# Optimization experiments

Hardware: AMD Instinct MI355X
Metric: run time of the kernel (lower is better)

The kernel has to match this reference:

```python
import jax, jax.numpy as jnp
import numpy as np

D_MODEL = 2048
N_HEADS = 16
N_KV = 4
HEAD_DIM = 128
SUB = 64
WINDOW = 512
THETA = 10000.0
NEG = jnp.float32(-1e30)


def _rope_tables(seq_len):
    inv_freq = 1.0 / (THETA ** (jnp.arange(0, HEAD_DIM, 2, dtype=jnp.float32) / HEAD_DIM))
    freqs = jnp.arange(seq_len, dtype=jnp.float32)[:, None] * inv_freq[None, :]  # [S, hd/2]
    emb = jnp.concatenate([freqs, freqs], axis=-1)  # [S, hd]
    return jnp.cos(emb), jnp.sin(emb)


def _rotate_half(x):
    x1, x2 = x[..., : HEAD_DIM // 2], x[..., HEAD_DIM // 2 :]
    return jnp.concatenate([-x2, x1], axis=-1)


def _apply_rope(t, cos, sin):
    # t: [B, H, S, hd]; cos/sin: [S, hd]
    c = cos[None, None]
    s = sin[None, None]
    return t * c + _rotate_half(t) * s


def setup_inputs() -> dict:
    key = jax.random.key(0)
    ks = jax.random.split(key, 6)
    B, S = 1, 2048
    std = 0.02
    return {
        "x": jax.random.normal(ks[0], (B, S, D_MODEL), dtype=jnp.float32),
        "Wq": jax.random.normal(ks[1], (D_MODEL, N_HEADS * HEAD_DIM), dtype=jnp.float32) * std,
        "Wk": jax.random.normal(ks[2], (D_MODEL, N_KV * HEAD_DIM), dtype=jnp.float32) * std,
        "Wv": jax.random.normal(ks[3], (D_MODEL, N_KV * HEAD_DIM), dtype=jnp.float32) * std,
        "Wo": jax.random.normal(ks[4], (N_HEADS * HEAD_DIM, D_MODEL), dtype=jnp.float32) * std,
        "lam": jnp.full((N_HEADS,), 0.1, dtype=jnp.float32),
    }


def reference(x, Wq, Wk, Wv, Wo, lam):
    B, S, _ = x.shape
    n_rep = N_HEADS // N_KV

    q = (x @ Wq).reshape(B, S, N_HEADS, HEAD_DIM).transpose(0, 2, 1, 3)  # [B,H,S,hd]
    k = (x @ Wk).reshape(B, S, N_KV, HEAD_DIM).transpose(0, 2, 1, 3)    # [B,KH,S,hd]
    v = (x @ Wv).reshape(B, S, N_KV, HEAD_DIM).transpose(0, 2, 1, 3)

    cos, sin = _rope_tables(S)
    q = _apply_rope(q, cos, sin)
    k = _apply_rope(k, cos, sin)

    # GQA repeat: each kv head replicated n_rep times consecutively
    k = jnp.repeat(k, n_rep, axis=1)  # [B,H,S,hd]
    v = jnp.repeat(v, n_rep, axis=1)

    q1, q2 = q[..., :SUB], q[..., SUB:]
    k1, k2 = k[..., :SUB], k[..., SUB:]
    scale = 1.0 / jnp.sqrt(jnp.float32(SUB))

    s1 = jnp.einsum("bhqd,bhkd->bhqk", q1, k1) * scale
    s2 = jnp.einsum("bhqd,bhkd->bhqk", q2, k2) * scale

    i = jnp.arange(S)[:, None]
    j = jnp.arange(S)[None, :]
    allowed = (j <= i) & (j >= i - WINDOW + 1)  # causal + sliding window
    s1 = jnp.where(allowed[None, None], s1, NEG)
    s2 = jnp.where(allowed[None, None], s2, NEG)

    a1 = jax.nn.softmax(s1.astype(jnp.float32), axis=-1).astype(x.dtype)
    a2 = jax.nn.softmax(s2.astype(jnp.float32), axis=-1).astype(x.dtype)

    diff = jax.nn.relu(a1 - lam[None, :, None, None] * a2)
    diff = diff / (jnp.sum(diff, axis=-1, keepdims=True) + 1e-6)

    out = jnp.einsum("bhqk,bhkd->bhqd", diff, v)  # [B,H,S,hd]
    out = out.transpose(0, 2, 1, 3).reshape(B, S, N_HEADS * HEAD_DIM)
    return out @ Wo
```

## Files before the change

kernel.cpp:

```cpp
#include <hip/hip_runtime.h>
#include <hip/hip_bf16.h>
#include <stdint.h>

typedef __attribute__((ext_vector_type(8))) short short8;
typedef __attribute__((ext_vector_type(4))) float f32x4;
using bf16 = __hip_bfloat16;

#define MFMA16(a, b, c) __builtin_amdgcn_mfma_f32_16x16x32_bf16((a), (b), (c), 0, 0, 0)

#define GLOAD_LDS16(g, l) __builtin_amdgcn_global_load_lds( \
    (const __attribute__((address_space(1))) void*)(g),     \
    (__attribute__((address_space(3))) void*)(l), 16, 0, 0)

__device__ __forceinline__ unsigned packbf2(float lo, float hi) {
  unsigned r;
  asm("v_cvt_pk_bf16_f32 %0, %1, %2" : "=v"(r) : "v"(lo), "v"(hi));
  return r;
}
__device__ __forceinline__ float ex2(float x) {
  float r;
  asm("v_exp_f32 %0, %1" : "=v"(r) : "v"(x));
  return r;
}
__device__ __forceinline__ float bflo(unsigned a) {
  union { unsigned u; float f; } v; v.u = a << 16; return v.f;
}
__device__ __forceinline__ float bfhi(unsigned a) {
  union { unsigned u; float f; } v; v.u = a & 0xFFFF0000u; return v.f;
}

template <bool EDGE, bool STORE>
__device__ __forceinline__ void p1v(const f32x4* s1v, const f32x4* s2v,
                                    float& l1, float& l2,
                                    int kb0, int myq, int lhi, int qrow,
                                    unsigned* Pt) {
  float sum1 = 0.f, sum2 = 0.f;
#pragma unroll
  for (int nt = 0; nt < 4; ++nt) {
#pragma unroll
    for (int r = 0; r < 4; ++r) {
      float e1 = ex2(s1v[nt][r]);
      float e2 = ex2(s2v[nt][r]);
      if (EDGE) {
        int key = kb0 + nt * 16 + lhi * 4 + r;
        bool ok = (key <= myq) && (key > myq - 512);
        e1 = ok ? e1 : 0.f;
        e2 = ok ? e2 : 0.f;
      }
      sum1 += e1; sum2 += e2;
      if (STORE)
        Pt[(nt * 16 + lhi * 4 + r) * 64 + qrow] = packbf2(e1, e2);
    }
  }
  l1 += sum1; l2 += sum2;
}

template <bool EDGE>
__device__ __forceinline__ float p2s(const f32x4* s1v, const f32x4* s2v,
                                     float c2, int kb0, int myq, int lhi, int l15,
                                     unsigned* pw) {
  float d0 = 0.f, d1 = 0.f;
#pragma unroll
  for (int nt = 0; nt < 4; ++nt) {
    float pr[4];
#pragma unroll
    for (int r = 0; r < 4; ++r) {
      float e1 = ex2(s1v[nt][r]);
      float e2 = ex2(s2v[nt][r]);
      float p = fmaf(-c2, e2, e1);
      p = fmaxf(p, 0.f);
      if (EDGE) {
        int key = kb0 + nt * 16 + lhi * 4 + r;
        bool ok = (key <= myq) && (key > myq - 512);
        p = ok ? p : 0.f;
      }
      pr[r] = p;
      if (r & 1) d1 += p; else d0 += p;
    }
    int pi = l15 * 36 + 8 * nt + 2 * lhi;
    pw[pi]     = packbf2(pr[0], pr[1]);
    pw[pi + 1] = packbf2(pr[2], pr[3]);
  }
  return d0 + d1;
}

__global__ __launch_bounds__(256) void prep_all(const float* __restrict__ x,
                                                const float* __restrict__ Wq,
                                                const float* __restrict__ Wk,
                                                const float* __restrict__ Wv,
                                                const float* __restrict__ Wo,
                                                bf16* __restrict__ xb,
                                                bf16* __restrict__ WqkvFT,
                                                bf16* __restrict__ WoFT)
{
  const int bx = blockIdx.x;
  const int tid = threadIdx.x;
  if (bx >= 80) {
    size_t i = ((size_t)(bx - 80) * 32 + blockIdx.y) * 2048 + tid * 8;
    const float* f = x + i;
    float4 a = *(const float4*)f;
    float4 b = *(const float4*)(f + 4);
    union { bf16 h[8]; short8 s; } u;
    u.h[0] = __float2bfloat16(a.x); u.h[1] = __float2bfloat16(a.y);
    u.h[2] = __float2bfloat16(a.z); u.h[3] = __float2bfloat16(a.w);
    u.h[4] = __float2bfloat16(b.x); u.h[5] = __float2bfloat16(b.y);
    u.h[6] = __float2bfloat16(b.z); u.h[7] = __float2bfloat16(b.w);
    *(short8*)(xb + i) = u.s;
    return;
  }
  const float* W;
  bf16* Wt;
  int N, n0, prm;
  if (bx < 32)      { W = Wq; Wt = WqkvFT; N = 2048; n0 = bx * 64;               prm = 1; }
  else if (bx < 40) { W = Wk; Wt = WqkvFT; N = 512;  n0 = 2048 + (bx - 32) * 64; prm = 1; }
  else if (bx < 48) { W = Wv; Wt = WqkvFT; N = 512;  n0 = 2560 + (bx - 40) * 64; prm = 0; }
  else              { W = Wo; Wt = WoFT;   N = 2048; n0 = (bx - 48) * 64;        prm = 0; }
  const int nloc0 = (N == 512) ? (n0 - ((n0 >= 2560) ? 2560 : 2048)) : ((bx < 32 || bx >= 48) ? (n0 & 2047) : 0);
  const int k0 = blockIdx.y * 64;

  __shared__ bf16 t[64][72];
#pragma unroll
  for (int pass = 0; pass < 4; ++pass) {
    int r = pass * 16 + (tid >> 4);
    int c = (tid & 15) * 4;
    float4 v = *(const float4*)(W + (size_t)(k0 + r) * N + nloc0 + c);
    t[c + 0][r] = __float2bfloat16(v.x);
    t[c + 1][r] = __float2bfloat16(v.y);
    t[c + 2][r] = __float2bfloat16(v.z);
    t[c + 3][r] = __float2bfloat16(v.w);
  }
  __syncthreads();
#pragma unroll
  for (int pass = 0; pass < 2; ++pass) {
    int n = pass * 32 + (tid >> 3);
    int k8 = (tid & 7) * 8;
    int ng = n0 + n;
    if (prm) {
      int d = ng & 127;
      int dp = (d & 31) | ((d & 32) << 1) | ((d & 64) >> 1);
      ng = (ng & ~127) | dp;
    }
    int frag = (ng >> 4) * 64 + ((k0 + k8) >> 5);
    int ln = (ng & 15) + 16 * ((k8 >> 3) & 3);
    *(short8*)(Wt + (size_t)frag * 512 + ln * 8) = *(const short8*)(&t[n][k8]);
  }
}

__global__ __launch_bounds__(512) void gemm_qkv(const bf16* __restrict__ A,
                                                const bf16* __restrict__ Bft,
                                                bf16* __restrict__ QKV,
                                                bf16* __restrict__ VTp,
                                                int M, int N, int K)
{
  __shared__ __align__(16) char smem[65536];
  bf16* As = (bf16*)smem;

  const int tid  = threadIdx.x;
  const int lane = tid & 63;
  const int w    = tid >> 6;
  const int wmg  = (w >> 2) * 4;
  const int wn3  = (w & 3) * 3;
  const int l15  = lane & 15;
  const int lhi  = lane >> 4;

  const int nbx = gridDim.x;
  const int lb  = blockIdx.y * nbx + blockIdx.x;
  const int nwg = nbx * gridDim.y;
  const int lsw = (lb & 7) * (nwg >> 3) + (lb >> 3);
  const int bm0 = (lsw / nbx) * 128;
  const int bn0 = (lsw % nbx) * 192;

  const int srow = tid >> 2;
  const int scol = ((tid & 3) ^ ((tid >> 3) & 3)) * 8;
  const int loff = l15 * 4 + (lhi ^ ((l15 >> 1) & 3));

  const int nkc = K >> 5;
  const bf16* bbase[3];
#pragma unroll
  for (int nt = 0; nt < 3; ++nt)
    bbase[nt] = Bft + ((size_t)((bn0 >> 4) + wn3 + nt) * nkc) * 512 + lane * 8;

  f32x4 acc[4][3];
  const f32x4 zero4 = {0.f, 0.f, 0.f, 0.f};
#pragma unroll
  for (int i = 0; i < 4; ++i)
#pragma unroll
    for (int j = 0; j < 3; ++j) acc[i][j] = zero4;

  short8 br0[3], br1[3], br2[3], br3[3];

#define GSTAGE_A(buf, kk)                                                           \
  { GLOAD_LDS16(A + (size_t)(bm0 + srow) * K + (kk) + scol,                         \
                As + (buf) * 4096 + tid * 8); }

#define BLOAD(breg, kc)                                                             \
  { _Pragma("unroll")                                                               \
    for (int nt = 0; nt < 3; ++nt) {                                                \
      asm volatile("global_load_dwordx4 %0, %1, off"                                \
                   : "=v"(breg[nt])                                                 \
                   : "v"(bbase[nt] + (size_t)(kc) * 512)                            \
                   : "memory");                                                     \
    } }

#define KSTEP(aslot, breg, wcn, ...)                                                \
  {                                                                                 \
    asm volatile("s_waitcnt vmcnt(" #wcn ")" ::: "memory");                         \
    __builtin_amdgcn_s_barrier();                                                   \
    __builtin_amdgcn_sched_barrier(0);                                              \
    __VA_ARGS__                                                                     \
    short8 a_[4];                                                                   \
    _Pragma("unroll")                                                               \
    for (int mt = 0; mt < 4; ++mt)                                                  \
      a_[mt] = *(const short8*)(As + (aslot) * 4096 + ((wmg + mt) * 64 + loff) * 8);\
    _Pragma("unroll")                                                               \
    for (int mt = 0; mt < 4; ++mt)                                                  \
      _Pragma("unroll")                                                             \
      for (int nt = 0; nt < 3; ++nt)                                                \
        acc[mt][nt] = MFMA16(a_[mt], breg[nt], acc[mt][nt]);                        \
  }

  GSTAGE_A(0, 0);  BLOAD(br0, 0);
  GSTAGE_A(1, 32); BLOAD(br1, 1);
  GSTAGE_A(2, 64); BLOAD(br2, 2);

  for (int t = 0; t < nkc - 4; t += 4) {
    KSTEP(0, br0, 8, GSTAGE_A(3, (t + 3) * 32); BLOAD(br3, t + 3);)
    KSTEP(1, br1, 8, GSTAGE_A(0, (t + 4) * 32); BLOAD(br0, t + 4);)
    KSTEP(2, br2, 8, GSTAGE_A(1, (t + 5) * 32); BLOAD(br1, t + 5);)
    KSTEP(3, br3, 8, GSTAGE_A(2, (t + 6) * 32); BLOAD(br2, t + 6);)
  }
  KSTEP(0, br0, 8, GSTAGE_A(3, (nkc - 1) * 32); BLOAD(br3, nkc - 1);)
  KSTEP(1, br1, 8, )
  KSTEP(2, br2, 4, )
  KSTEP(3, br3, 0, )
#undef GSTAGE_A
#undef BLOAD
#undef KSTEP

  __syncthreads();

  const int ropeW = (bn0 + 192 <= 2560) ? 192 : ((bn0 >= 2560) ? 0 : 64);

  if (ropeW > 0) {
    float* Lf = (float*)smem;
#pragma unroll
    for (int half = 0; half < 2; ++half) {
      if ((w >> 2) == half) {
#pragma unroll
        for (int mt = 0; mt < 4; ++mt)
#pragma unroll
          for (int nt = 0; nt < 3; ++nt) {
            int lc = (wn3 + nt) * 16 + l15;
            if (lc < ropeW) {
#pragma unroll
              for (int r = 0; r < 4; ++r)
                Lf[(mt * 16 + lhi * 4 + r) * ropeW + lc] = acc[mt][nt][r];
            }
          }
      }
      __syncthreads();
      {
        int row = tid >> 3;
        int s = bm0 + half * 64 + row;
        if (ropeW == 192) {
          int cg = (tid & 7) * 24;
          bf16* orow = QKV + (size_t)s * 3072 + bn0 + cg;
          union { bf16 h[24]; short8 v[3]; } o;
#pragma unroll
          for (int e = 0; e < 24; ++e) {
            int c = cg + e;
            int g = bn0 + c;
            int p = g & 127;
            int w32 = p & 63;
            int b = p >> 6;
            int d = b * 32 + (w32 & 31);
            float scale = (g < 2048) ? 0.180336880111120f : 1.0f;
            float inv = __expf(-(float)d * (9.210340371976184f / 64.0f));
            float ang = (float)s * inv;
            float cs = __cosf(ang), sn = __sinf(ang);
            bool first = (w32 < 32);
            float xa = Lf[row * 192 + c];
            float xb2 = Lf[row * 192 + (first ? c + 32 : c - 32)];
            float out = fmaf(first ? -xb2 : xb2, sn, xa * cs);
            o.h[e] = __float2bfloat16(out * scale);
          }
          *(short8*)(orow)      = o.v[0];
          *(short8*)(orow + 8)  = o.v[1];
          *(short8*)(orow + 16) = o.v[2];
        } else {
          int cg = (tid & 7) * 8;
          bf16* orow = QKV + (size_t)s * 3072 + bn0 + cg;
          union { bf16 h[8]; short8 v; } o;
#pragma unroll
          for (int e = 0; e < 8; ++e) {
            int c = cg + e;
            int g = bn0 + c;
            int p = g & 127;
            int w32 = p & 63;
            int b = p >> 6;
            int d = b * 32 + (w32 & 31);
            float inv = __expf(-(float)d * (9.210340371976184f / 64.0f));
            float ang = (float)s * inv;
            float cs = __cosf(ang), sn = __sinf(ang);
            bool first = (w32 < 32);
            float xa = Lf[row * 64 + c];
            float xb2 = Lf[row * 64 + (first ? c + 32 : c - 32)];
            float out = fmaf(first ? -xb2 : xb2, sn, xa * cs);
            o.h[e] = __float2bfloat16(out);
          }
          *(short8*)(orow) = o.v;
        }
      }
      __syncthreads();
    }
  }
  if (bn0 + 192 > 2560) {
#pragma unroll
    for (int nt = 0; nt < 3; ++nt) {
      int gfc = bn0 + (wn3 + nt) * 16;
      if (gfc >= 2560) {
        int dim = gfc - 2560 + l15;
#pragma unroll
        for (int mt = 0; mt < 4; ++mt) {
          int key0 = bm0 + (w >> 2) * 64 + mt * 16 + lhi * 4;
          uint2 pk;
          pk.x = packbf2(acc[mt][nt][0], acc[mt][nt][1]);
          pk.y = packbf2(acc[mt][nt][2], acc[mt][nt][3]);
          *(uint2*)(VTp + (size_t)dim * 2048 + key0) = pk;
        }
      }
    }
  }
}

__global__ __launch_bounds__(512) void gemm_wo(const bf16* __restrict__ A,
                                               const bf16* __restrict__ Bft,
                                               float* __restrict__ C,
                                               int M, int N, int K)
{
  __shared__ __align__(16) bf16 As[4 * 4096];

  const int tid  = threadIdx.x;
  const int lane = tid & 63;
  const int w    = tid >> 6;
  const int wmg  = (w >> 2) * 4;
  const int wn2  = (w & 3) * 2;
  const int l15  = lane & 15;
  const int lhi  = lane >> 4;

  const int nbx = gridDim.x;
  const int lb  = blockIdx.y * nbx + blockIdx.x;
  const int nwg = nbx * gridDim.y;
  const int lsw = (lb & 7) * (nwg >> 3) + (lb >> 3);
  const int bm0 = (lsw / nbx) * 128;
  const int bn0 = (lsw % nbx) * 128;

  const int srow = tid >> 2;
  const int scol = ((tid & 3) ^ ((tid >> 3) & 3)) * 8;
  const int loff = l15 * 4 + (lhi ^ ((l15 >> 1) & 3));

  const int nkc = K >> 5;
  const bf16* bbase[2];
#pragma unroll
  for (int nt = 0; nt < 2; ++nt)
    bbase[nt] = Bft + ((size_t)((bn0 >> 4) + wn2 + nt) * nkc) * 512 + lane * 8;

  f32x4 acc[4][2];
  const f32x4 zero4 = {0.f, 0.f, 0.f, 0.f};
#pragma unroll
  for (int i = 0; i < 4; ++i)
#pragma unroll
    for (int j = 0; j < 2; ++j) acc[i][j] = zero4;

  short8 br0[2], br1[2], br2[2], br3[2];

#define GSTAGE_A(buf, kk)                                                           \
  { GLOAD_LDS16(A + (size_t)(bm0 + srow) * K + (kk) + scol,                         \
                As + (buf) * 4096 + tid * 8); }

#define BLOAD(breg, kc)                                                             \
  { _Pragma("unroll")                                                               \
    for (int nt = 0; nt < 2; ++nt) {                                                \
      asm volatile("global_load_dwordx4 %0, %1, off"                                \
                   : "=v"(breg[nt])                                                 \
                   : "v"(bbase[nt] + (size_t)(kc) * 512)                            \
                   : "memory");                                                     \
    } }

#define KSTEP(aslot, breg, wcn, ...)                                                \
  {                                                                                 \
    asm volatile("s_waitcnt vmcnt(" #wcn ")" ::: "memory");                         \
    __builtin_amdgcn_s_barrier();                                                   \
    __builtin_amdgcn_sched_barrier(0);                                              \
    __VA_ARGS__                                                                     \
    short8 a_[4];                                                                   \
    _Pragma("unroll")                                                               \
    for (int mt = 0; mt < 4; ++mt)                                                  \
      a_[mt] = *(const short8*)(As + (aslot) * 4096 + ((wmg + mt) * 64 + loff) * 8);\
    _Pragma("unroll")                                                               \
    for (int mt = 0; mt < 4; ++mt)                                                  \
      _Pragma("unroll")                                                             \
      for (int nt = 0; nt < 2; ++nt)                                                \
        acc[mt][nt] = MFMA16(a_[mt], breg[nt], acc[mt][nt]);                        \
  }

  GSTAGE_A(0, 0);  BLOAD(br0, 0);
  GSTAGE_A(1, 32); BLOAD(br1, 1);
  GSTAGE_A(2, 64); BLOAD(br2, 2);

  for (int t = 0; t < nkc - 4; t += 4) {
    KSTEP(0, br0, 6, GSTAGE_A(3, (t + 3) * 32); BLOAD(br3, t + 3);)
    KSTEP(1, br1, 6, GSTAGE_A(0, (t + 4) * 32); BLOAD(br0, t + 4);)
    KSTEP(2, br2, 6, GSTAGE_A(1, (t + 5) * 32); BLOAD(br1, t + 5);)
    KSTEP(3, br3, 6, GSTAGE_A(2, (t + 6) * 32); BLOAD(br2, t + 6);)
  }
  KSTEP(0, br0, 6, GSTAGE_A(3, (nkc - 1) * 32); BLOAD(br3, nkc - 1);)
  KSTEP(1, br1, 6, )
  KSTEP(2, br2, 3, )
  KSTEP(3, br3, 0, )
#undef GSTAGE_A
#undef BLOAD
#undef KSTEP

#pragma unroll
  for (int mt = 0; mt < 4; ++mt) {
    int row0 = bm0 + (wmg + mt) * 16 + lhi * 4;
#pragma unroll
    for (int nt = 0; nt < 2; ++nt) {
      int col = bn0 + (w & 3) * 32 + nt * 16 + l15;
#pragma unroll
      for (int r = 0; r < 4; ++r)
        C[(size_t)(row0 + r) * N + col] = acc[mt][nt][r];
    }
  }
}

__global__ __launch_bounds__(256) void diff_attn(const bf16* __restrict__ QKV,
                                                 const bf16* __restrict__ VT,
                                                 const float* __restrict__ lam,
                                                 bf16* __restrict__ O,
                                                 unsigned* __restrict__ PA,
                                                 unsigned* __restrict__ PB)
{
  __shared__ __align__(16) bf16 Kb[2][64 * 128];
  __shared__ __align__(16) bf16 Vb[2][128 * 64];
  __shared__ __align__(16) bf16 Pw[4][16 * 72];

  const int lb  = blockIdx.y * 32 + blockIdx.x;
  const int lsw = (lb & 7) * 64 + (lb >> 3);
  const int qb  = lsw & 31;
  const int h   = lsw >> 5;

  const int kvh  = h >> 2;
  const int tid  = threadIdx.x;
  const int lane = tid & 63;
  const int w    = tid >> 6;
  const int l15  = lane & 15;
  const int lhi  = lane >> 4;
  const int qg   = qb * 64 + w * 16;
  const int myq  = qg + l15;
  const int qrow = w * 16 + l15;
  const float lamv = lam[h];

  unsigned* Pbase = (lsw < 160) ? (PA + (size_t)lsw * 32768)
                                : (PB + (size_t)(lsw - 160) * 32768);

  const bf16* Kg = QKV + 2048 + (size_t)kvh * 128;
  const bf16* Vg = VT + (size_t)kvh * 128 * 2048;

  short8 qf[4];
  {
    const bf16* qrowp = QKV + (size_t)myq * 3072 + h * 128;
#pragma unroll
    for (int c = 0; c < 4; ++c)
      qf[c] = *(const short8*)(qrowp + c * 32 + lhi * 8);
  }

  const int t0 = (qb >= 8) ? (qb - 8) : 0;

#define STAGE_K(buf, kbase)                                                     \
  {                                                                             \
    _Pragma("unroll")                                                           \
    for (int p = 0; p < 4; ++p) {                                               \
      int c = p * 256 + tid;                                                    \
      int r = c >> 4, q = c & 15;                                               \
      GLOAD_LDS16(Kg + (size_t)((kbase) + r) * 3072 + ((q ^ (r & 7)) * 8),      \
                  &Kb[buf][c * 8]);                                             \
    }                                                                           \
  }
#define STAGE_V(buf, kbase)                                                     \
  {                                                                             \
    _Pragma("unroll")                                                           \
    for (int p = 0; p < 4; ++p) {                                               \
      int c = p * 256 + tid;                                                    \
      int d = c >> 3, q = c & 7;                                                \
      GLOAD_LDS16(Vg + (size_t)d * 2048 + (kbase) + ((q ^ (d & 7)) * 8),        \
                  &Vb[buf][c * 8]);                                             \
    }                                                                           \
  }
#define KFRAG(buf, nt, qc) \
  (*(const short8*)(&Kb[buf][(((nt) * 16 + l15) * 16 + ((qc) ^ (((nt) * 16 + l15) & 7))) * 8]))
#define VFRAG(buf, n, qc) \
  (*(const short8*)(&Vb[buf][(((n) * 16 + l15) * 8 + ((qc) ^ (((n) * 16 + l15) & 7))) * 8]))
#define QK_TILE(cur)                                            \
  _Pragma("unroll")                                             \
  for (int nt = 0; nt < 4; ++nt) {                              \
    f32x4 s1 = zero4, s2 = zero4;                               \
    s1 = MFMA16(KFRAG(cur, nt, lhi),      qf[0], s1);           \
    s1 = MFMA16(KFRAG(cur, nt, 8 + lhi),  qf[2], s1);           \
    s2 = MFMA16(KFRAG(cur, nt, 4 + lhi),  qf[1], s2);           \
    s2 = MFMA16(KFRAG(cur, nt, 12 + lhi), qf[3], s2);           \
    s1v[nt] = s1; s2v[nt] = s2;                                 \
  }

  const f32x4 zero4 = {0.f, 0.f, 0.f, 0.f};

  float l1 = 0.f, l2 = 0.f;
  STAGE_K(0, t0 * 64);
  asm volatile("s_waitcnt vmcnt(0)" ::: "memory");
  __builtin_amdgcn_s_barrier();
  {
    int cur = 0;
    for (int t = t0; t <= qb; ++t, cur ^= 1) {
      if (t < qb) {
        STAGE_K(cur ^ 1, (t + 1) * 64);
        asm volatile("s_waitcnt vmcnt(4)" ::: "memory");
      } else {
        asm volatile("s_waitcnt vmcnt(0)" ::: "memory");
      }
      __builtin_amdgcn_s_barrier();
      __builtin_amdgcn_sched_barrier(0);
      const int kb0 = t * 64;
      f32x4 s1v[4], s2v[4];
      QK_TILE(cur);
      unsigned* Pt = Pbase + (size_t)(t - t0) * 4096;
      if (t == qb) {
        p1v<true, false>(s1v, s2v, l1, l2, kb0, myq, lhi, qrow, nullptr);
      } else if (qb >= 8 && t == t0) {
        p1v<true, true>(s1v, s2v, l1, l2, kb0, myq, lhi, qrow, Pt);
      } else {
        p1v<false, true>(s1v, s2v, l1, l2, kb0, myq, lhi, qrow, Pt);
      }
      __builtin_amdgcn_s_barrier();
    }
  }

  l1 += __shfl_xor(l1, 16, 64);
  l1 += __shfl_xor(l1, 32, 64);
  l2 += __shfl_xor(l2, 16, 64);
  l2 += __shfl_xor(l2, 32, 64);
  const float c2 = lamv * l1 / l2;

  f32x4 accv[8];
#pragma unroll
  for (int n = 0; n < 8; ++n) accv[n] = zero4;
  float dln = 0.f;

  STAGE_V(0, qb * 64);
  STAGE_K(0, qb * 64);
  asm volatile("s_waitcnt vmcnt(0)" ::: "memory");
  __builtin_amdgcn_s_barrier();
  if (qb > t0) STAGE_V(1, (qb - 1) * 64);
  {
    const int kb0 = qb * 64;
    unsigned* pw = (unsigned*)&Pw[w][0];
    f32x4 s1v[4], s2v[4];
    QK_TILE(0);
    dln += p2s<true>(s1v, s2v, c2, kb0, myq, lhi, l15, pw);
#pragma unroll
    for (int kc = 0; kc < 2; ++kc) {
      short8 pa2 = *(const short8*)(&Pw[w][l15 * 72 + kc * 32 + lhi * 8]);
#pragma unroll
      for (int n = 0; n < 8; ++n)
        accv[n] = MFMA16(pa2, VFRAG(0, n, kc * 4 + lhi), accv[n]);
    }
  }
  __builtin_amdgcn_s_barrier();
  {
    int cur = 1;
    for (int t = qb - 1; t >= t0; --t, cur ^= 1) {
      const unsigned* Pt = Pbase + (size_t)(t - t0) * 4096 + qrow;
      unsigned pv[16];
#pragma unroll
      for (int kc = 0; kc < 2; ++kc)
#pragma unroll
        for (int j = 0; j < 8; ++j)
          pv[kc * 8 + j] = Pt[(kc * 32 + lhi * 8 + j) * 64];
      if (t > t0) {
        STAGE_V(cur ^ 1, (t - 1) * 64);
        asm volatile("s_waitcnt vmcnt(4)" ::: "memory");
      } else {
        asm volatile("s_waitcnt vmcnt(0)" ::: "memory");
      }
      __builtin_amdgcn_s_barrier();
      __builtin_amdgcn_sched_barrier(0);
      short8 pa[2];
      float dl = 0.f;
#pragma unroll
      for (int kc = 0; kc < 2; ++kc) {
        union { unsigned u[4]; short8 s; } pk;
#pragma unroll
        for (int jp = 0; jp < 4; ++jp) {
          unsigned a = pv[kc * 8 + 2 * jp];
          unsigned b = pv[kc * 8 + 2 * jp + 1];
          float p0 = fmaxf(fmaf(-c2, bfhi(a), bflo(a)), 0.f);
          float p1 = fmaxf(fmaf(-c2, bfhi(b), bflo(b)), 0.f);
          dl += p0 + p1;
          pk.u[jp] = packbf2(p0, p1);
        }
        pa[kc] = pk.s;
      }
      dln += dl;
#pragma unroll
      for (int kc = 0; kc < 2; ++kc)
#pragma unroll
        for (int n = 0; n < 8; ++n)
          accv[n] = MFMA16(pa[kc], VFRAG(cur, n, kc * 4 + lhi), accv[n]);
      __builtin_amdgcn_s_barrier();
    }
  }

  dln += __shfl_xor(dln, 16, 64);
  dln += __shfl_xor(dln, 32, 64);

#pragma unroll
  for (int r = 0; r < 4; ++r) {
    int srcq = lhi * 4 + r;
    int src = (lane & 48) | srcq;
    float dq = __shfl(dln, src, 64);
    float lq = __shfl(l1, src, 64);
    float rinv = 1.f / (dq + lq * 1e-6f);
    int qo = qg + srcq;
#pragma unroll
    for (int n = 0; n < 8; ++n) {
      O[(size_t)qo * 2048 + h * 128 + n * 16 + l15] =
          __float2bfloat16(accv[n][r] * rinv);
    }
  }
#undef STAGE_K
#undef STAGE_V
#undef KFRAG
#undef VFRAG
#undef QK_TILE
}

extern "C" void kernel_launch(void* const* d_in, const int* in_sizes, int n_in,
                              void* d_out, int out_size, void* d_ws, size_t ws_size,
                              hipStream_t stream)
{
  const float* x   = (const float*)d_in[0];
  const float* Wq  = (const float*)d_in[1];
  const float* Wk  = (const float*)d_in[2];
  const float* Wv  = (const float*)d_in[3];
  const float* Wo  = (const float*)d_in[4];
  const float* lam = (const float*)d_in[5];

  char* ws = (char*)d_ws;
  bf16* xb     = (bf16*)(ws);
  bf16* WqkvFT = (bf16*)(ws + 8ull  * (1u << 20));
  bf16* WoFT   = (bf16*)(ws + 20ull * (1u << 20));
  bf16* QKV    = (bf16*)(ws + 28ull * (1u << 20));
  bf16* ATT    = (bf16*)(ws + 40ull * (1u << 20));
  bf16* VT     = (bf16*)(ws + 48ull * (1u << 20));
  unsigned* PA = (unsigned*)(ws);
  unsigned* PB = (unsigned*)(ws + 50ull * (1u << 20));

  prep_all<<<dim3(144, 32), 256, 0, stream>>>(x, Wq, Wk, Wv, Wo, xb, WqkvFT, WoFT);
  gemm_qkv<<<dim3(16, 16), 512, 0, stream>>>(xb, WqkvFT, QKV, VT, 2048, 3072, 2048);
  diff_attn<<<dim3(32, 16), 256, 0, stream>>>(QKV, VT, lam, ATT, PA, PB);
  gemm_wo<<<dim3(16, 16), 512, 0, stream>>>(ATT, WoFT, (float*)d_out, 2048, 2048, 2048);
}
```

Before: 102.4 us.

## Cache only the last four probability tiles and recompute older ones in pass two

```diff
diff --git a/kernel.cpp b/kernel.cpp
--- a/kernel.cpp
+++ b/kernel.cpp
@@ -439,8 +439,7 @@
                                                  const bf16* __restrict__ VT,
                                                  const float* __restrict__ lam,
                                                  bf16* __restrict__ O,
-                                                 unsigned* __restrict__ PA,
-                                                 unsigned* __restrict__ PB)
+                                                 unsigned* __restrict__ P)
 {
   __shared__ __align__(16) bf16 Kb[2][64 * 128];
   __shared__ __align__(16) bf16 Vb[2][128 * 64];
@@ -462,8 +461,7 @@
   const int qrow = w * 16 + l15;
   const float lamv = lam[h];
 
-  unsigned* Pbase = (lsw < 160) ? (PA + (size_t)lsw * 32768)
-                                : (PB + (size_t)(lsw - 160) * 32768);
+  unsigned* Pbase = P + (size_t)lsw * 16384;
 
   const bf16* Kg = QKV + 2048 + (size_t)kvh * 128;
   const bf16* Vg = VT + (size_t)kvh * 128 * 2048;
@@ -533,13 +531,15 @@
       const int kb0 = t * 64;
       f32x4 s1v[4], s2v[4];
       QK_TILE(cur);
-      unsigned* Pt = Pbase + (size_t)(t - t0) * 4096;
       if (t == qb) {
         p1v<true, false>(s1v, s2v, l1, l2, kb0, myq, lhi, qrow, nullptr);
+      } else if (t > qb - 5) {
+        unsigned* Pt = Pbase + (size_t)(t - qb + 4) * 4096;
+        p1v<false, true>(s1v, s2v, l1, l2, kb0, myq, lhi, qrow, Pt);
       } else if (qb >= 8 && t == t0) {
-        p1v<true, true>(s1v, s2v, l1, l2, kb0, myq, lhi, qrow, Pt);
+        p1v<true, false>(s1v, s2v, l1, l2, kb0, myq, lhi, qrow, nullptr);
       } else {
-        p1v<false, true>(s1v, s2v, l1, l2, kb0, myq, lhi, qrow, Pt);
+        p1v<false, false>(s1v, s2v, l1, l2, kb0, myq, lhi, qrow, nullptr);
       }
       __builtin_amdgcn_s_barrier();
     }
@@ -555,6 +555,8 @@
 #pragma unroll
   for (int n = 0; n < 8; ++n) accv[n] = zero4;
   float dln = 0.f;
+
+  const int tcEnd = (qb - 4 > t0) ? (qb - 4) : t0;
 
   STAGE_V(0, qb * 64);
   STAGE_K(0, qb * 64);
@@ -576,48 +578,81 @@
     }
   }
   __builtin_amdgcn_s_barrier();
-  {
-    int cur = 1;
-    for (int t = qb - 1; t >= t0; --t, cur ^= 1) {
-      const unsigned* Pt = Pbase + (size_t)(t - t0) * 4096 + qrow;
-      unsigned pv[16];
-#pragma unroll
-      for (int kc = 0; kc < 2; ++kc)
-#pragma unroll
-        for (int j = 0; j < 8; ++j)
-          pv[kc * 8 + j] = Pt[(kc * 32 + lhi * 8 + j) * 64];
-      if (t > t0) {
-        STAGE_V(cur ^ 1, (t - 1) * 64);
+
+  for (int t = qb - 1; t >= tcEnd; --t) {
+    const unsigned* Pt = Pbase + (size_t)(t - qb + 4) * 4096 + qrow;
+    unsigned pv[16];
+#pragma unroll
+    for (int kc = 0; kc < 2; ++kc)
+#pragma unroll
+      for (int j = 0; j < 8; ++j)
+        pv[kc * 8 + j] = Pt[(kc * 32 + lhi * 8 + j) * 64];
+    const int vb = (qb - t) & 1;
+    const bool haveNext = (t - 1 >= t0);
+    const bool nextRecomp = haveNext && (t - 1 < tcEnd);
+    if (haveNext) {
+      STAGE_V((qb - (t - 1)) & 1, (t - 1) * 64);
+      if (nextRecomp) {
+        STAGE_K((qb - (t - 1)) & 1, (t - 1) * 64);
+        asm volatile("s_waitcnt vmcnt(8)" ::: "memory");
+      } else {
         asm volatile("s_waitcnt vmcnt(4)" ::: "memory");
-      } else {
-        asm volatile("s_waitcnt vmcnt(0)" ::: "memory");
-      }
-      __builtin_amdgcn_s_barrier();
-      __builtin_amdgcn_sched_barrier(0);
-      short8 pa[2];
-      float dl = 0.f;
-#pragma unroll
-      for (int kc = 0; kc < 2; ++kc) {
-        union { unsigned u[4]; short8 s; } pk;
-#pragma unroll
-        for (int jp = 0; jp < 4; ++jp) {
-          unsigned a = pv[kc * 8 + 2 * jp];
-          unsigned b = pv[kc * 8 + 2 * jp + 1];
-          float p0 = fmaxf(fmaf(-c2, bfhi(a), bflo(a)), 0.f);
-          float p1 = fmaxf(fmaf(-c2, bfhi(b), bflo(b)), 0.f);
-          dl += p0 + p1;
-          pk.u[jp] = packbf2(p0, p1);
-        }
-        pa[kc] = pk.s;
-      }
-      dln += dl;
-#pragma unroll
-      for (int kc = 0; kc < 2; ++kc)
-#pragma unroll
-        for (int n = 0; n < 8; ++n)
-          accv[n] = MFMA16(pa[kc], VFRAG(cur, n, kc * 4 + lhi), accv[n]);
-      __builtin_amdgcn_s_barrier();
-    }
+      }
+    } else {
+      asm volatile("s_waitcnt vmcnt(0)" ::: "memory");
+    }
+    __builtin_amdgcn_s_barrier();
+    __builtin_amdgcn_sched_barrier(0);
+    short8 pa[2];
+    float dl = 0.f;
+#pragma unroll
+    for (int kc = 0; kc < 2; ++kc) {
+      union { unsigned u[4]; short8 s; } pk;
+#pragma unroll
+      for (int jp = 0; jp < 4; ++jp) {
+        unsigned a = pv[kc * 8 + 2 * jp];
+        unsigned b = pv[kc * 8 + 2 * jp + 1];
+        float p0 = fmaxf(fmaf(-c2, bfhi(a), bflo(a)), 0.f);
+        float p1 = fmaxf(fmaf(-c2, bfhi(b), bflo(b)), 0.f);
+        dl += p0 + p1;
+        pk.u[jp] = packbf2(p0, p1);
+      }
+      pa[kc] = pk.s;
+    }
+    dln += dl;
+#pragma unroll
+    for (int kc = 0; kc < 2; ++kc)
+#pragma unroll
+      for (int n = 0; n < 8; ++n)
+        accv[n] = MFMA16(pa[kc], VFRAG(vb, n, kc * 4 + lhi), accv[n]);
+    __builtin_amdgcn_s_barrier();
+  }
+
+  for (int t = tcEnd - 1; t >= t0; --t) {
+    const int vb = (qb - t) & 1;
+    if (t - 1 >= t0) {
+      STAGE_V((qb - (t - 1)) & 1, (t - 1) * 64);
+      STAGE_K((qb - (t - 1)) & 1, (t - 1) * 64);
+      asm volatile("s_waitcnt vmcnt(8)" ::: "memory");
+    } else {
+      asm volatile("s_waitcnt vmcnt(0)" ::: "memory");
+    }
+    __builtin_amdgcn_s_barrier();
+    __builtin_amdgcn_sched_barrier(0);
+    const int kb0 = t * 64;
+    unsigned* pw = (unsigned*)&Pw[w][0];
+    f32x4 s1v[4], s2v[4];
+    QK_TILE(vb);
+    if (qb >= 8 && t == t0) dln += p2s<true>(s1v, s2v, c2, kb0, myq, lhi, l15, pw);
+    else                    dln += p2s<false>(s1v, s2v, c2, kb0, myq, lhi, l15, pw);
+#pragma unroll
+    for (int kc = 0; kc < 2; ++kc) {
+      short8 pa2 = *(const short8*)(&Pw[w][l15 * 72 + kc * 32 + lhi * 8]);
+#pragma unroll
+      for (int n = 0; n < 8; ++n)
+        accv[n] = MFMA16(pa2, VFRAG(vb, n, kc * 4 + lhi), accv[n]);
+    }
+    __builtin_amdgcn_s_barrier();
   }
 
   dln += __shfl_xor(dln, 16, 64);
@@ -662,11 +697,10 @@
   bf16* QKV    = (bf16*)(ws + 28ull * (1u << 20));
   bf16* ATT    = (bf16*)(ws + 40ull * (1u << 20));
   bf16* VT     = (bf16*)(ws + 48ull * (1u << 20));
-  unsigned* PA = (unsigned*)(ws);
-  unsigned* PB = (unsigned*)(ws + 50ull * (1u << 20));
+  unsigned* P  = (unsigned*)(ws + 50ull * (1u << 20));
 
   prep_all<<<dim3(144, 32), 256, 0, stream>>>(x, Wq, Wk, Wv, Wo, xb, WqkvFT, WoFT);
   gemm_qkv<<<dim3(16, 16), 512, 0, stream>>>(xb, WqkvFT, QKV, VT, 2048, 3072, 2048);
-  diff_attn<<<dim3(32, 16), 256, 0, stream>>>(QKV, VT, lam, ATT, PA, PB);
+  diff_attn<<<dim3(32, 16), 256, 0, stream>>>(QKV, VT, lam, ATT, P);
   gemm_wo<<<dim3(16, 16), 512, 0, stream>>>(ATT, WoFT, (float*)d_out, 2048, 2048, 2048);
 }
```

Measured after the change: 104.1 us. About the same (+1.7%).
